# Optimization experiments

Hardware: AMD Instinct MI355X
Metric: run time of the kernel (lower is better)

Reference implementation:

```python
import jax, jax.numpy as jnp
import numpy as np

B, N, C = 2, 2048, 256
L, H = 4, 4
HD = C // H  # 64, div=1 so q/k keep full head dim
EPS = 1e-5   # BatchNorm eps (eval mode, running_mean=0, running_var=1)


def setup_inputs() -> dict:
    key = jax.random.key(0)
    ks = jax.random.split(key, 20)
    w = lambda k, s: jax.random.normal(k, s, jnp.float32) * 0.05
    return {
        'x': jax.random.normal(ks[0], (B, N, C), jnp.float32),
        'in_w1': w(ks[1], (C, C)), 'in_b1': w(ks[2], (C,)),
        'in_g1': 1.0 + w(ks[3], (C,)), 'in_be1': w(ks[4], (C,)),
        'in_w2': w(ks[5], (C, C)), 'in_b2': w(ks[6], (C,)),
        'in_g2': 1.0 + w(ks[7], (C,)), 'in_be2': w(ks[8], (C,)),
        'q_w': w(ks[9], (L, H, HD, HD)), 'k_w': w(ks[10], (L, H, HD, HD)),
        'v_w': w(ks[11], (L, H, HD, HD)), 'v_b': w(ks[12], (L, H, HD)),
        't_w': w(ks[13], (L, H, HD, HD)), 't_b': w(ks[14], (L, H, HD)),
        'bn_g': 1.0 + w(ks[15], (L, H, HD)), 'bn_b': w(ks[16], (L, H, HD)),
        'proj_w': w(ks[17], (L, C, C)), 'proj_b': w(ks[18], (L, C)),
    }


def _bn(t, g, b):
    # eval-mode BatchNorm1d with running_mean=0, running_var=1
    return t * (g / jnp.sqrt(1.0 + EPS))[:, None] + b[:, None]


def _forward(x, in_w1, in_b1, in_g1, in_be1, in_w2, in_b2, in_g2, in_be2,
             q_w, k_w, v_w, v_b, t_w, t_b, bn_g, bn_b, proj_w, proj_b):
    Bq, Nq, Cq = x.shape
    h = x.transpose(0, 2, 1)  # (B, C, N)
    h = jax.nn.relu(_bn(jnp.einsum('oc,bcn->bon', in_w1, h) + in_b1[:, None], in_g1, in_be1))
    h = jax.nn.relu(_bn(jnp.einsum('oc,bcn->bon', in_w2, h) + in_b2[:, None], in_g2, in_be2))
    h = h.reshape(Bq, H, HD, Nq)  # split heads (B, H, hd, N)
    for l in range(L):
        xq = jnp.einsum('hoc,bhcn->bhno', q_w[l], h)                       # (B,H,N,hd)
        xk = jnp.einsum('hoc,bhcn->bhon', k_w[l], h)                       # (B,H,hd,N)
        xv = jnp.einsum('hoc,bhcn->bhon', v_w[l], h) + v_b[l][None, :, :, None]
        attn = jax.nn.softmax(jnp.einsum('bhno,bhom->bhnm', xq, xk), axis=-1)
        # offset-attention normalization: divide by column sums (torch dim=1)
        attn = attn / (1e-9 + attn.sum(axis=2, keepdims=True))
        xr = jnp.einsum('bhcn,bhnm->bhcm', xv, attn)                       # (B,H,hd,N)
        d = h - xr
        t = jnp.einsum('hoc,bhcn->bhon', t_w[l], d) + t_b[l][None, :, :, None]
        xr = jax.nn.relu(t * (bn_g[l] / jnp.sqrt(1.0 + EPS))[None, :, :, None]
                         + bn_b[l][None, :, :, None])
        h = h + xr
        hm = h.reshape(Bq, Cq, Nq)  # concat heads
        hm = jnp.einsum('oc,bcn->bon', proj_w[l], hm) + proj_b[l][:, None]
        h = hm.reshape(Bq, H, HD, Nq)
    return h.reshape(Bq, Cq, Nq).transpose(0, 2, 1)  # (B, N, C)


def reference(x, in_w1, in_b1, in_g1, in_be1, in_w2, in_b2, in_g2, in_be2,
              q_w, k_w, v_w, v_b, t_w, t_b, bn_g, bn_b, proj_w, proj_b):
    return _forward(x, in_w1, in_b1, in_g1, in_be1, in_w2, in_b2, in_g2, in_be2,
                    q_w, k_w, v_w, v_b, t_w, t_b, bn_g, bn_b, proj_w, proj_b)
```

## Files before the change

### kernel.cpp

```cpp
#include <hip/hip_runtime.h>
#include <math.h>

constexpr int NB = 2, NN = 2048, NC = 256, NL = 4, NH = 4, ND = 64;
constexpr float EPSV = 1e-5f;

using half8 = __attribute__((ext_vector_type(8))) _Float16;
using half4 = __attribute__((ext_vector_type(4))) _Float16;
using f32x4 = __attribute__((ext_vector_type(4))) float;

__device__ __forceinline__ f32x4 mfma16(half8 a, half8 b, f32x4 c) {
    return __builtin_amdgcn_mfma_f32_16x16x32_f16(a, b, c, 0, 0, 0);
}

template<int EPI, bool INF16>
__global__ __launch_bounds__(256) void gemm_mfma(
    const float* __restrict__ Wg, const float* __restrict__ bias,
    const float* __restrict__ gam, const float* __restrict__ bet,
    const void* __restrict__ inp, _Float16* __restrict__ out16)
{
    int b = blockIdx.x, o0 = blockIdx.y * 64, n0 = blockIdx.z * 64;
    __shared__ __align__(16) _Float16 Wlds[64][264];
    int t = threadIdx.x;
    for (int r = 0; r < 32; ++r) {
        int id = r * 256 + t;
        int o = id >> 7, k2 = id & 127;
        float2 wv = *(const float2*)(Wg + (size_t)(o0 + o) * NC + 2 * k2);
        Wlds[o][2 * k2]     = (_Float16)wv.x;
        Wlds[o][2 * k2 + 1] = (_Float16)wv.y;
    }
    __syncthreads();
    int w = t >> 6, li = t & 15, qd = (t >> 4) & 3;
    f32x4 acc[4];
#pragma unroll
    for (int g = 0; g < 4; ++g) acc[g] = {0.f, 0.f, 0.f, 0.f};
#pragma unroll
    for (int ks = 0; ks < 8; ++ks) {
        half8 a = *(const half8*)&Wlds[w * 16 + li][ks * 32 + qd * 8];
#pragma unroll
        for (int g = 0; g < 4; ++g) {
            int n = n0 + g * 16 + li;
            half8 bf;
            if (INF16) {
                bf = *(const half8*)((const _Float16*)inp +
                        ((size_t)(b * NN + n) * NC + ks * 32 + qd * 8));
            } else {
                const float* xp = (const float*)inp +
                        ((size_t)(b * NN + n) * NC + ks * 32 + qd * 8);
                float4 x0 = *(const float4*)xp, x1 = *(const float4*)(xp + 4);
                bf[0]=(_Float16)x0.x; bf[1]=(_Float16)x0.y; bf[2]=(_Float16)x0.z; bf[3]=(_Float16)x0.w;
                bf[4]=(_Float16)x1.x; bf[5]=(_Float16)x1.y; bf[6]=(_Float16)x1.z; bf[7]=(_Float16)x1.w;
            }
            acc[g] = mfma16(a, bf, acc[g]);
        }
    }
    int ob = o0 + w * 16 + qd * 4;
    float4 bs = *(const float4*)(bias + ob);
    float4 gs = {0,0,0,0}, be = {0,0,0,0};
    if (EPI == 1) { gs = *(const float4*)(gam + ob); be = *(const float4*)(bet + ob); }
    float scl = rsqrtf(1.f + EPSV);
#pragma unroll
    for (int g = 0; g < 4; ++g) {
        int n = n0 + g * 16 + li;
        half4 hv;
#pragma unroll
        for (int r = 0; r < 4; ++r) {
            float v = acc[g][r] + ((const float*)&bs)[r];
            if (EPI == 1)
                v = fmaxf(0.f, v * (((const float*)&gs)[r] * scl) + ((const float*)&be)[r]);
            hv[r] = (_Float16)v;
        }
        *(half4*)(out16 + (size_t)(b * NN + n) * NC + ob) = hv;
    }
}

__global__ __launch_bounds__(256) void qkv_mfma(
    const float* __restrict__ qw, const float* __restrict__ kw,
    const float* __restrict__ vw, const float* __restrict__ vb,
    const _Float16* __restrict__ h16, _Float16* __restrict__ q16,
    _Float16* __restrict__ k16, _Float16* __restrict__ v16, int l)
{
    int bh = blockIdx.x, n0 = blockIdx.y * 64, z = blockIdx.z;
    int hh = bh & 3, b = bh >> 2;
    const float* wp = (z == 0 ? qw : (z == 1 ? kw : vw)) + (size_t)(l * NH + hh) * ND * ND;
    __shared__ __align__(16) _Float16 Wlds[64][72];
    int t = threadIdx.x;
    for (int r = 0; r < 8; ++r) {
        int id = r * 256 + t;
        int o = id >> 5, k2 = id & 31;
        float2 wv = *(const float2*)(wp + (size_t)o * ND + 2 * k2);
        Wlds[o][2 * k2]     = (_Float16)wv.x;
        Wlds[o][2 * k2 + 1] = (_Float16)wv.y;
    }
    __syncthreads();
    int w = t >> 6, li = t & 15, qd = (t >> 4) & 3;
    f32x4 acc[4];
#pragma unroll
    for (int g = 0; g < 4; ++g) acc[g] = {0.f, 0.f, 0.f, 0.f};
#pragma unroll
    for (int ks = 0; ks < 2; ++ks) {
        half8 a = *(const half8*)&Wlds[w * 16 + li][ks * 32 + qd * 8];
#pragma unroll
        for (int g = 0; g < 4; ++g) {
            int n = n0 + g * 16 + li;
            half8 bf = *(const half8*)(h16 +
                    ((size_t)(b * NN + n) * NC + hh * 64 + ks * 32 + qd * 8));
            acc[g] = mfma16(a, bf, acc[g]);
        }
    }
    int ob = w * 16 + qd * 4;
    if (z < 2) {
        _Float16* outp = (z == 0 ? q16 : k16) + (size_t)bh * NN * ND;
#pragma unroll
        for (int g = 0; g < 4; ++g) {
            int n = n0 + g * 16 + li;
            half4 hv;
#pragma unroll
            for (int r = 0; r < 4; ++r) hv[r] = (_Float16)acc[g][r];
            *(half4*)(outp + (size_t)n * ND + ob) = hv;
        }
    } else {
        float4 vb4 = *(const float4*)(vb + (size_t)(l * NH + hh) * ND + ob);
        _Float16* outp = v16 + (size_t)bh * ND * NN;
#pragma unroll
        for (int g = 0; g < 4; ++g) {
            int n = n0 + g * 16 + li;
#pragma unroll
            for (int r = 0; r < 4; ++r)
                outp[(size_t)(ob + r) * NN + n] = (_Float16)(acc[g][r] + ((const float*)&vb4)[r]);
        }
    }
}

__global__ __launch_bounds__(256) void rowsum_kernel(
    const _Float16* __restrict__ qh, const _Float16* __restrict__ kh,
    float* __restrict__ rowsum)
{
    int bh = blockIdx.x, nt = blockIdx.y, ms = blockIdx.z;
    const _Float16* qp = qh + (size_t)bh * NN * ND;
    const _Float16* kp = kh + (size_t)bh * NN * ND;
    int t = threadIdx.x, w = t >> 6, li = t & 15, qd = (t >> 4) & 3;
    int nr = nt * 64 + w * 16;
    half8 aq0 = *(const half8*)(qp + (size_t)(nr + li) * ND + qd * 8);
    half8 aq1 = *(const half8*)(qp + (size_t)(nr + li) * ND + qd * 8 + 32);
    float rsacc[4] = {0.f, 0.f, 0.f, 0.f};
    for (int it = 0; it < 8; ++it) {
        int m0 = ms * 512 + it * 64;
        f32x4 s[4];
#pragma unroll
        for (int g = 0; g < 4; ++g) {
            const _Float16* kb = kp + (size_t)(m0 + g * 16 + li) * ND + qd * 8;
            half8 b0 = *(const half8*)(kb);
            half8 b1 = *(const half8*)(kb + 32);
            s[g] = {0.f, 0.f, 0.f, 0.f};
            s[g] = mfma16(aq0, b0, s[g]);
            s[g] = mfma16(aq1, b1, s[g]);
        }
#pragma unroll
        for (int r = 0; r < 4; ++r)
            rsacc[r] += __expf(s[0][r]) + __expf(s[1][r]) + __expf(s[2][r]) + __expf(s[3][r]);
    }
#pragma unroll
    for (int r = 0; r < 4; ++r) {
        float v = rsacc[r];
        v += __shfl_xor(v, 1); v += __shfl_xor(v, 2);
        v += __shfl_xor(v, 4); v += __shfl_xor(v, 8);
        if (li == 0) atomicAdd(&rowsum[bh * NN + nr + qd * 4 + r], v);
    }
}

__global__ __launch_bounds__(256) void attn_mfma_kernel(
    const _Float16* __restrict__ qh, const _Float16* __restrict__ kh,
    const _Float16* __restrict__ vh, const float* __restrict__ rowsum,
    float* __restrict__ xrp, float* __restrict__ csp)
{
    int bh = blockIdx.x, m0 = blockIdx.y * 64, ns = blockIdx.z;
    const _Float16* qp = qh + (size_t)bh * NN * ND;
    const _Float16* kp = kh + (size_t)bh * NN * ND;
    const _Float16* vp = vh + (size_t)bh * ND * NN;
    __shared__ __align__(16) _Float16 Plds[64 * 72];
    __shared__ float cs_wave[4][64];
    int t = threadIdx.x, w = t >> 6, li = t & 15, qd = (t >> 4) & 3;
    half8 bk[4][2];
#pragma unroll
    for (int g = 0; g < 4; ++g) {
        const _Float16* kb = kp + (size_t)(m0 + g * 16 + li) * ND + qd * 8;
        bk[g][0] = *(const half8*)(kb);
        bk[g][1] = *(const half8*)(kb + 32);
    }
    f32x4 acc[4];
#pragma unroll
    for (int g = 0; g < 4; ++g) acc[g] = {0.f, 0.f, 0.f, 0.f};
    float csacc[4] = {0.f, 0.f, 0.f, 0.f};
    for (int it = 0; it < 16; ++it) {
        int n0 = ns * 1024 + it * 64;
        const _Float16* qrow = qp + (size_t)(n0 + w * 16 + li) * ND + qd * 8;
        half8 aq0 = *(const half8*)(qrow);
        half8 aq1 = *(const half8*)(qrow + 32);
        f32x4 s[4];
#pragma unroll
        for (int g = 0; g < 4; ++g) {
            s[g] = {0.f, 0.f, 0.f, 0.f};
            s[g] = mfma16(aq0, bk[g][0], s[g]);
            s[g] = mfma16(aq1, bk[g][1], s[g]);
        }
        float irs[4];
#pragma unroll
        for (int r = 0; r < 4; ++r)
            irs[r] = 1.0f / rowsum[bh * NN + n0 + w * 16 + qd * 4 + r];
#pragma unroll
        for (int g = 0; g < 4; ++g) {
            half4 pv; float lsum = 0.f;
#pragma unroll
            for (int r = 0; r < 4; ++r) {
                float p = __expf(s[g][r]) * irs[r];
                lsum += p;
                pv[r] = (_Float16)p;
            }
            csacc[g] += lsum;
            *(half4*)(&Plds[(g * 16 + li) * 72 + w * 16 + qd * 4]) = pv;
        }
        __syncthreads();
        const _Float16* vrow = vp + (size_t)(w * 16 + li) * NN + n0 + qd * 8;
        half8 av0 = *(const half8*)(vrow);
        half8 av1 = *(const half8*)(vrow + 32);
#pragma unroll
        for (int g = 0; g < 4; ++g) {
            half8 b0 = *(const half8*)(&Plds[(g * 16 + li) * 72 + qd * 8]);
            half8 b1 = *(const half8*)(&Plds[(g * 16 + li) * 72 + qd * 8 + 32]);
            acc[g] = mfma16(av0, b0, acc[g]);
            acc[g] = mfma16(av1, b1, acc[g]);
        }
        __syncthreads();
    }
#pragma unroll
    for (int g = 0; g < 4; ++g) {
        float v = csacc[g];
        v += __shfl_xor(v, 16); v += __shfl_xor(v, 32);
        if (qd == 0) cs_wave[w][g * 16 + li] = v;
    }
    __syncthreads();
    if (t < 64) {
        float cs = cs_wave[0][t] + cs_wave[1][t] + cs_wave[2][t] + cs_wave[3][t];
        csp[((size_t)ns * NB * NH + bh) * NN + m0 + t] = cs;
    }
    float* xo = xrp + (size_t)ns * ((size_t)NB * NC * NN);
#pragma unroll
    for (int g = 0; g < 4; ++g)
#pragma unroll
        for (int r = 0; r < 4; ++r)
            xo[(size_t)(bh * 64 + w * 16 + qd * 4 + r) * NN + m0 + g * 16 + li] = acc[g][r];
}

__global__ __launch_bounds__(256) void fuse_dx(
    const float* __restrict__ xrp, const float* __restrict__ csp,
    const _Float16* __restrict__ h16, _Float16* __restrict__ d16)
{
    int bh = blockIdx.x, n0 = blockIdx.y * 32, c0g = blockIdx.z * 32;
    int b = bh >> 2, cbase = (bh & 3) * 64 + c0g;
    __shared__ float ts[32][33];
    int t = threadIdx.x, xcol = t & 31, yr = t >> 5;
    int m = n0 + xcol;
    float icv = 1.f / (1e-9f + csp[(size_t)bh * NN + m] + csp[(size_t)NB * NH * NN + bh * NN + m]);
#pragma unroll
    for (int r = 0; r < 4; ++r) {
        int c = yr + 8 * r;
        size_t off = (size_t)(bh * 64 + c0g + c) * NN + m;
        ts[c][xcol] = (xrp[off] + xrp[(size_t)NB * NC * NN + off]) * icv;
    }
    __syncthreads();
#pragma unroll
    for (int r = 0; r < 4; ++r) {
        int n = n0 + yr + 8 * r;
        size_t off = (size_t)(b * NN + n) * NC + cbase + xcol;
        d16[off] = (_Float16)((float)h16[off] - ts[xcol][yr + 8 * r]);
    }
}

__global__ __launch_bounds__(256) void delta_mfma(
    const float* __restrict__ tw, const float* __restrict__ tb,
    const float* __restrict__ bng, const float* __restrict__ bnb,
    const _Float16* __restrict__ h16, const _Float16* __restrict__ d16,
    _Float16* __restrict__ hn16, int l)
{
    int bh = blockIdx.x, n0 = blockIdx.y * 64;
    int hh = bh & 3, b = bh >> 2;
    const float* wp = tw + (size_t)(l * NH + hh) * ND * ND;
    __shared__ __align__(16) _Float16 Wlds[64][72];
    int t = threadIdx.x;
    for (int r = 0; r < 8; ++r) {
        int id = r * 256 + t;
        int o = id >> 5, k2 = id & 31;
        float2 wv = *(const float2*)(wp + (size_t)o * ND + 2 * k2);
        Wlds[o][2 * k2]     = (_Float16)wv.x;
        Wlds[o][2 * k2 + 1] = (_Float16)wv.y;
    }
    __syncthreads();
    int w = t >> 6, li = t & 15, qd = (t >> 4) & 3;
    f32x4 acc[4];
#pragma unroll
    for (int g = 0; g < 4; ++g) acc[g] = {0.f, 0.f, 0.f, 0.f};
#pragma unroll
    for (int ks = 0; ks < 2; ++ks) {
        half8 a = *(const half8*)&Wlds[w * 16 + li][ks * 32 + qd * 8];
#pragma unroll
        for (int g = 0; g < 4; ++g) {
            int n = n0 + g * 16 + li;
            half8 bf = *(const half8*)(d16 +
                    ((size_t)(b * NN + n) * NC + hh * 64 + ks * 32 + qd * 8));
            acc[g] = mfma16(a, bf, acc[g]);
        }
    }
    int ob = w * 16 + qd * 4;
    float4 tb4 = *(const float4*)(tb  + (size_t)(l * NH + hh) * ND + ob);
    float4 g4  = *(const float4*)(bng + (size_t)(l * NH + hh) * ND + ob);
    float4 b4  = *(const float4*)(bnb + (size_t)(l * NH + hh) * ND + ob);
    float scl = rsqrtf(1.f + EPSV);
#pragma unroll
    for (int g = 0; g < 4; ++g) {
        int n = n0 + g * 16 + li;
        size_t off = (size_t)(b * NN + n) * NC + hh * 64 + ob;
        half4 h4 = *(const half4*)(h16 + off);
        half4 hv;
#pragma unroll
        for (int r = 0; r < 4; ++r) {
            float tv = acc[g][r] + ((const float*)&tb4)[r];
            float x2 = fmaxf(0.f, tv * (((const float*)&g4)[r] * scl) + ((const float*)&b4)[r]);
            hv[r] = (_Float16)((float)h4[r] + x2);
        }
        *(half4*)(hn16 + off) = hv;
    }
}

__global__ __launch_bounds__(256) void final_out(
    const _Float16* __restrict__ h16, float* __restrict__ out)
{
    size_t e = ((size_t)blockIdx.x * 256 + threadIdx.x) * 4;
    half4 hv = *(const half4*)(h16 + e);
    float4 o;
    o.x = (float)hv[0]; o.y = (float)hv[1]; o.z = (float)hv[2]; o.w = (float)hv[3];
    *(float4*)(out + e) = o;
}

extern "C" void kernel_launch(void* const* d_in, const int* in_sizes, int n_in,
                              void* d_out, int out_size, void* d_ws, size_t ws_size,
                              hipStream_t stream)
{
    (void)in_sizes; (void)n_in; (void)out_size; (void)ws_size;
    const float* x      = (const float*)d_in[0];
    const float* in_w1  = (const float*)d_in[1];
    const float* in_b1  = (const float*)d_in[2];
    const float* in_g1  = (const float*)d_in[3];
    const float* in_be1 = (const float*)d_in[4];
    const float* in_w2  = (const float*)d_in[5];
    const float* in_b2  = (const float*)d_in[6];
    const float* in_g2  = (const float*)d_in[7];
    const float* in_be2 = (const float*)d_in[8];
    const float* q_w    = (const float*)d_in[9];
    const float* k_w    = (const float*)d_in[10];
    const float* v_w    = (const float*)d_in[11];
    const float* v_b    = (const float*)d_in[12];
    const float* t_w    = (const float*)d_in[13];
    const float* t_b    = (const float*)d_in[14];
    const float* bn_g   = (const float*)d_in[15];
    const float* bn_b   = (const float*)d_in[16];
    const float* proj_w = (const float*)d_in[17];
    const float* proj_b = (const float*)d_in[18];

    float* ws = (float*)d_ws;
    const size_t M = (size_t)NB * NC * NN;
    float* xrp    = ws;
    float* rowsum = ws + 2 * M;
    float* csp    = rowsum + (size_t)NB * NH * NN;
    _Float16* hbase = (_Float16*)(ws + 2 * M + 65536);
    _Float16* h16  = hbase;
    _Float16* hA16 = hbase + M;
    _Float16* d16  = hbase + 2 * M;
    _Float16* q16  = hbase + 3 * M;
    _Float16* k16  = hbase + 4 * M;
    _Float16* v16  = hbase + 5 * M;

    dim3 g1(NB, NC / 64, NN / 64);

    gemm_mfma<1, false><<<g1, 256, 0, stream>>>(in_w1, in_b1, in_g1, in_be1, x,    hA16);
    gemm_mfma<1, true ><<<g1, 256, 0, stream>>>(in_w2, in_b2, in_g2, in_be2, hA16, h16);

    for (int l = 0; l < NL; l++) {
        hipMemsetAsync(rowsum, 0, (size_t)NB * NH * NN * sizeof(float), stream);
        qkv_mfma<<<dim3(NB * NH, NN / 64, 3), 256, 0, stream>>>(
            q_w, k_w, v_w, v_b, h16, q16, k16, v16, l);
        rowsum_kernel<<<dim3(NB * NH, NN / 64, 4), 256, 0, stream>>>(q16, k16, rowsum);
        attn_mfma_kernel<<<dim3(NB * NH, NN / 64, 2), 256, 0, stream>>>(
            q16, k16, v16, rowsum, xrp, csp);
        fuse_dx<<<dim3(NB * NH, NN / 32, 2), 256, 0, stream>>>(xrp, csp, h16, d16);
        delta_mfma<<<dim3(NB * NH, NN / 64), 256, 0, stream>>>(
            t_w, t_b, bn_g, bn_b, h16, d16, hA16, l);
        gemm_mfma<0, true><<<g1, 256, 0, stream>>>(proj_w + (size_t)l * NC * NC,
                                                   proj_b + (size_t)l * NC,
                                                   nullptr, nullptr, hA16, h16);
    }

    final_out<<<dim3(M / 1024), 256, 0, stream>>>(h16, (float*)d_out);
}
```

Measured before the change: 454.6 us.

## Load weights directly to registers, halve GEMM tiles, double-buffer attention P tile

The GEMM, QKV and delta kernels no longer stage weights through LDS with a barrier. Each lane now loads its A fragments straight from global memory into registers and converts them to fp16. The channel GEMM and delta kernels drop from 64 to 32 columns per block, doubling the grid to improve occupancy across CUs. The attention kernel double-buffers the P tile in LDS so it can drop one __syncthreads per iteration, and it loads rowsum as a float4. The risks are redundant global weight reads across blocks and a possible race: with two buffers and only one barrier per iteration, iteration it+2 writes the buffer that iteration it reads.

```diff
diff --git a/kernel.cpp b/kernel.cpp
--- a/kernel.cpp
+++ b/kernel.cpp
@@ -10,6 +10,13 @@
 
 __device__ __forceinline__ f32x4 mfma16(half8 a, half8 b, f32x4 c) {
     return __builtin_amdgcn_mfma_f32_16x16x32_f16(a, b, c, 0, 0, 0);
+}
+__device__ __forceinline__ half8 cvt8(const float* p) {
+    float4 x0 = *(const float4*)p, x1 = *(const float4*)(p + 4);
+    half8 h;
+    h[0]=(_Float16)x0.x; h[1]=(_Float16)x0.y; h[2]=(_Float16)x0.z; h[3]=(_Float16)x0.w;
+    h[4]=(_Float16)x1.x; h[5]=(_Float16)x1.y; h[6]=(_Float16)x1.z; h[7]=(_Float16)x1.w;
+    return h;
 }
 
 template<int EPI, bool INF16>
@@ -18,39 +25,27 @@
     const float* __restrict__ gam, const float* __restrict__ bet,
     const void* __restrict__ inp, _Float16* __restrict__ out16)
 {
-    int b = blockIdx.x, o0 = blockIdx.y * 64, n0 = blockIdx.z * 64;
-    __shared__ __align__(16) _Float16 Wlds[64][264];
-    int t = threadIdx.x;
-    for (int r = 0; r < 32; ++r) {
-        int id = r * 256 + t;
-        int o = id >> 7, k2 = id & 127;
-        float2 wv = *(const float2*)(Wg + (size_t)(o0 + o) * NC + 2 * k2);
-        Wlds[o][2 * k2]     = (_Float16)wv.x;
-        Wlds[o][2 * k2 + 1] = (_Float16)wv.y;
-    }
-    __syncthreads();
-    int w = t >> 6, li = t & 15, qd = (t >> 4) & 3;
-    f32x4 acc[4];
-#pragma unroll
-    for (int g = 0; g < 4; ++g) acc[g] = {0.f, 0.f, 0.f, 0.f};
+    int b = blockIdx.x, o0 = blockIdx.y * 64, n0 = blockIdx.z * 32;
+    int t = threadIdx.x, w = t >> 6, li = t & 15, qd = (t >> 4) & 3;
+    const float* wr = Wg + (size_t)(o0 + w * 16 + li) * NC + qd * 8;
+    half8 af[8];
+#pragma unroll
+    for (int ks = 0; ks < 8; ++ks) af[ks] = cvt8(wr + ks * 32);
+    f32x4 acc[2];
+    acc[0] = {0.f, 0.f, 0.f, 0.f}; acc[1] = {0.f, 0.f, 0.f, 0.f};
 #pragma unroll
     for (int ks = 0; ks < 8; ++ks) {
-        half8 a = *(const half8*)&Wlds[w * 16 + li][ks * 32 + qd * 8];
-#pragma unroll
-        for (int g = 0; g < 4; ++g) {
+#pragma unroll
+        for (int g = 0; g < 2; ++g) {
             int n = n0 + g * 16 + li;
             half8 bf;
             if (INF16) {
                 bf = *(const half8*)((const _Float16*)inp +
                         ((size_t)(b * NN + n) * NC + ks * 32 + qd * 8));
             } else {
-                const float* xp = (const float*)inp +
-                        ((size_t)(b * NN + n) * NC + ks * 32 + qd * 8);
-                float4 x0 = *(const float4*)xp, x1 = *(const float4*)(xp + 4);
-                bf[0]=(_Float16)x0.x; bf[1]=(_Float16)x0.y; bf[2]=(_Float16)x0.z; bf[3]=(_Float16)x0.w;
-                bf[4]=(_Float16)x1.x; bf[5]=(_Float16)x1.y; bf[6]=(_Float16)x1.z; bf[7]=(_Float16)x1.w;
+                bf = cvt8((const float*)inp + ((size_t)(b * NN + n) * NC + ks * 32 + qd * 8));
             }
-            acc[g] = mfma16(a, bf, acc[g]);
+            acc[g] = mfma16(af[ks], bf, acc[g]);
         }
     }
     int ob = o0 + w * 16 + qd * 4;
@@ -59,7 +54,7 @@
     if (EPI == 1) { gs = *(const float4*)(gam + ob); be = *(const float4*)(bet + ob); }
     float scl = rsqrtf(1.f + EPSV);
 #pragma unroll
-    for (int g = 0; g < 4; ++g) {
+    for (int g = 0; g < 2; ++g) {
         int n = n0 + g * 16 + li;
         half4 hv;
 #pragma unroll
@@ -82,30 +77,20 @@
     int bh = blockIdx.x, n0 = blockIdx.y * 64, z = blockIdx.z;
     int hh = bh & 3, b = bh >> 2;
     const float* wp = (z == 0 ? qw : (z == 1 ? kw : vw)) + (size_t)(l * NH + hh) * ND * ND;
-    __shared__ __align__(16) _Float16 Wlds[64][72];
-    int t = threadIdx.x;
-    for (int r = 0; r < 8; ++r) {
-        int id = r * 256 + t;
-        int o = id >> 5, k2 = id & 31;
-        float2 wv = *(const float2*)(wp + (size_t)o * ND + 2 * k2);
-        Wlds[o][2 * k2]     = (_Float16)wv.x;
-        Wlds[o][2 * k2 + 1] = (_Float16)wv.y;
-    }
-    __syncthreads();
-    int w = t >> 6, li = t & 15, qd = (t >> 4) & 3;
+    int t = threadIdx.x, w = t >> 6, li = t & 15, qd = (t >> 4) & 3;
+    const float* wr = wp + (size_t)(w * 16 + li) * ND + qd * 8;
+    half8 af0 = cvt8(wr), af1 = cvt8(wr + 32);
     f32x4 acc[4];
 #pragma unroll
     for (int g = 0; g < 4; ++g) acc[g] = {0.f, 0.f, 0.f, 0.f};
 #pragma unroll
-    for (int ks = 0; ks < 2; ++ks) {
-        half8 a = *(const half8*)&Wlds[w * 16 + li][ks * 32 + qd * 8];
-#pragma unroll
-        for (int g = 0; g < 4; ++g) {
-            int n = n0 + g * 16 + li;
-            half8 bf = *(const half8*)(h16 +
-                    ((size_t)(b * NN + n) * NC + hh * 64 + ks * 32 + qd * 8));
-            acc[g] = mfma16(a, bf, acc[g]);
-        }
+    for (int g = 0; g < 4; ++g) {
+        int n = n0 + g * 16 + li;
+        const _Float16* hb = h16 + ((size_t)(b * NN + n) * NC + hh * 64 + qd * 8);
+        half8 b0 = *(const half8*)(hb);
+        half8 b1 = *(const half8*)(hb + 32);
+        acc[g] = mfma16(af0, b0, acc[g]);
+        acc[g] = mfma16(af1, b1, acc[g]);
     }
     int ob = w * 16 + qd * 4;
     if (z < 2) {
@@ -177,7 +162,7 @@
     const _Float16* qp = qh + (size_t)bh * NN * ND;
     const _Float16* kp = kh + (size_t)bh * NN * ND;
     const _Float16* vp = vh + (size_t)bh * ND * NN;
-    __shared__ __align__(16) _Float16 Plds[64 * 72];
+    __shared__ __align__(16) _Float16 Plds[2][64 * 72];
     __shared__ float cs_wave[4][64];
     int t = threadIdx.x, w = t >> 6, li = t & 15, qd = (t >> 4) & 3;
     half8 bk[4][2];
@@ -193,6 +178,7 @@
     float csacc[4] = {0.f, 0.f, 0.f, 0.f};
     for (int it = 0; it < 16; ++it) {
         int n0 = ns * 1024 + it * 64;
+        _Float16* Pb = Plds[it & 1];
         const _Float16* qrow = qp + (size_t)(n0 + w * 16 + li) * ND + qd * 8;
         half8 aq0 = *(const half8*)(qrow);
         half8 aq1 = *(const half8*)(qrow + 32);
@@ -203,10 +189,8 @@
             s[g] = mfma16(aq0, bk[g][0], s[g]);
             s[g] = mfma16(aq1, bk[g][1], s[g]);
         }
-        float irs[4];
-#pragma unroll
-        for (int r = 0; r < 4; ++r)
-            irs[r] = 1.0f / rowsum[bh * NN + n0 + w * 16 + qd * 4 + r];
+        float4 rs4 = *(const float4*)(rowsum + bh * NN + n0 + w * 16 + qd * 4);
+        float irs[4] = {1.f / rs4.x, 1.f / rs4.y, 1.f / rs4.z, 1.f / rs4.w};
 #pragma unroll
         for (int g = 0; g < 4; ++g) {
             half4 pv; float lsum = 0.f;
@@ -217,7 +201,7 @@
                 pv[r] = (_Float16)p;
             }
             csacc[g] += lsum;
-            *(half4*)(&Plds[(g * 16 + li) * 72 + w * 16 + qd * 4]) = pv;
+            *(half4*)(&Pb[(g * 16 + li) * 72 + w * 16 + qd * 4]) = pv;
         }
         __syncthreads();
         const _Float16* vrow = vp + (size_t)(w * 16 + li) * NN + n0 + qd * 8;
@@ -225,12 +209,11 @@
         half8 av1 = *(const half8*)(vrow + 32);
 #pragma unroll
         for (int g = 0; g < 4; ++g) {
-            half8 b0 = *(const half8*)(&Plds[(g * 16 + li) * 72 + qd * 8]);
-            half8 b1 = *(const half8*)(&Plds[(g * 16 + li) * 72 + qd * 8 + 32]);
+            half8 b0 = *(const half8*)(&Pb[(g * 16 + li) * 72 + qd * 8]);
+            half8 b1 = *(const half8*)(&Pb[(g * 16 + li) * 72 + qd * 8 + 32]);
             acc[g] = mfma16(av0, b0, acc[g]);
             acc[g] = mfma16(av1, b1, acc[g]);
         }
-        __syncthreads();
     }
 #pragma unroll
     for (int g = 0; g < 4; ++g) {
@@ -282,33 +265,22 @@
     const _Float16* __restrict__ h16, const _Float16* __restrict__ d16,
     _Float16* __restrict__ hn16, int l)
 {
-    int bh = blockIdx.x, n0 = blockIdx.y * 64;
+    int bh = blockIdx.x, n0 = blockIdx.y * 32;
     int hh = bh & 3, b = bh >> 2;
     const float* wp = tw + (size_t)(l * NH + hh) * ND * ND;
-    __shared__ __align__(16) _Float16 Wlds[64][72];
-    int t = threadIdx.x;
-    for (int r = 0; r < 8; ++r) {
-        int id = r * 256 + t;
-        int o = id >> 5, k2 = id & 31;
-        float2 wv = *(const float2*)(wp + (size_t)o * ND + 2 * k2);
-        Wlds[o][2 * k2]     = (_Float16)wv.x;
-        Wlds[o][2 * k2 + 1] = (_Float16)wv.y;
-    }
-    __syncthreads();
-    int w = t >> 6, li = t & 15, qd = (t >> 4) & 3;
-    f32x4 acc[4];
-#pragma unroll
-    for (int g = 0; g < 4; ++g) acc[g] = {0.f, 0.f, 0.f, 0.f};
-#pragma unroll
-    for (int ks = 0; ks < 2; ++ks) {
-        half8 a = *(const half8*)&Wlds[w * 16 + li][ks * 32 + qd * 8];
-#pragma unroll
-        for (int g = 0; g < 4; ++g) {
-            int n = n0 + g * 16 + li;
-            half8 bf = *(const half8*)(d16 +
-                    ((size_t)(b * NN + n) * NC + hh * 64 + ks * 32 + qd * 8));
-            acc[g] = mfma16(a, bf, acc[g]);
-        }
+    int t = threadIdx.x, w = t >> 6, li = t & 15, qd = (t >> 4) & 3;
+    const float* wr = wp + (size_t)(w * 16 + li) * ND + qd * 8;
+    half8 af0 = cvt8(wr), af1 = cvt8(wr + 32);
+    f32x4 acc[2];
+    acc[0] = {0.f, 0.f, 0.f, 0.f}; acc[1] = {0.f, 0.f, 0.f, 0.f};
+#pragma unroll
+    for (int g = 0; g < 2; ++g) {
+        int n = n0 + g * 16 + li;
+        const _Float16* db = d16 + ((size_t)(b * NN + n) * NC + hh * 64 + qd * 8);
+        half8 b0 = *(const half8*)(db);
+        half8 b1 = *(const half8*)(db + 32);
+        acc[g] = mfma16(af0, b0, acc[g]);
+        acc[g] = mfma16(af1, b1, acc[g]);
     }
     int ob = w * 16 + qd * 4;
     float4 tb4 = *(const float4*)(tb  + (size_t)(l * NH + hh) * ND + ob);
@@ -316,7 +288,7 @@
     float4 b4  = *(const float4*)(bnb + (size_t)(l * NH + hh) * ND + ob);
     float scl = rsqrtf(1.f + EPSV);
 #pragma unroll
-    for (int g = 0; g < 4; ++g) {
+    for (int g = 0; g < 2; ++g) {
         int n = n0 + g * 16 + li;
         size_t off = (size_t)(b * NN + n) * NC + hh * 64 + ob;
         half4 h4 = *(const half4*)(h16 + off);
@@ -379,7 +351,7 @@
     _Float16* k16  = hbase + 4 * M;
     _Float16* v16  = hbase + 5 * M;
 
-    dim3 g1(NB, NC / 64, NN / 64);
+    dim3 g1(NB, NC / 64, NN / 32);
 
     gemm_mfma<1, false><<<g1, 256, 0, stream>>>(in_w1, in_b1, in_g1, in_be1, x,    hA16);
     gemm_mfma<1, true ><<<g1, 256, 0, stream>>>(in_w2, in_b2, in_g2, in_be2, hA16, h16);
@@ -392,7 +364,7 @@
         attn_mfma_kernel<<<dim3(NB * NH, NN / 64, 2), 256, 0, stream>>>(
             q16, k16, v16, rowsum, xrp, csp);
         fuse_dx<<<dim3(NB * NH, NN / 32, 2), 256, 0, stream>>>(xrp, csp, h16, d16);
-        delta_mfma<<<dim3(NB * NH, NN / 64), 256, 0, stream>>>(
+        delta_mfma<<<dim3(NB * NH, NN / 32), 256, 0, stream>>>(
             t_w, t_b, bn_g, bn_b, h16, d16, hA16, l);
         gemm_mfma<0, true><<<g1, 256, 0, stream>>>(proj_w + (size_t)l * NC * NC,
                                                    proj_b + (size_t)l * NC,
```

Result: slower. 465.1 us (+2.3%).
